# Kernel optimization log

Hardware: AMD Instinct MI355X
Metric: run time of the kernel (lower is better)

The kernel has to match this reference:

```python
import jax, jax.numpy as jnp
import numpy as np

EMBED = 1024
HEAD = 128

def setup_inputs() -> dict:
    key = jax.random.key(0)
    k1, k2, k3, k4 = jax.random.split(key, 4)
    x = jax.random.normal(k1, (4, 4096, EMBED), dtype=jnp.float32)
    # nn.Linear default init ~ U(-1/sqrt(fan_in), 1/sqrt(fan_in)); weights stored as [in, out] for x @ W
    s = 1.0 / np.sqrt(EMBED)
    Wq = jax.random.uniform(k2, (EMBED, HEAD), dtype=jnp.float32, minval=-s, maxval=s)
    Wk = jax.random.uniform(k3, (EMBED, HEAD), dtype=jnp.float32, minval=-s, maxval=s)
    Wv = jax.random.uniform(k4, (EMBED, HEAD), dtype=jnp.float32, minval=-s, maxval=s)
    return {"x": x, "Wq": Wq, "Wk": Wk, "Wv": Wv}

def reference(x, Wq, Wk, Wv):
    # x: [B, S, E]
    B, S, E = x.shape
    q = x @ Wq  # [B, S, H]
    k = x @ Wk
    v = x @ Wv
    scale = jnp.asarray(k.shape[-1], x.dtype) ** -0.5
    scores = jnp.einsum('bqh,bkh->bqk', q, k) * scale  # [B, S, S]
    causal = jnp.tril(jnp.ones((S, S), dtype=bool))
    scores = jnp.where(causal, scores, jnp.asarray(-jnp.inf, x.dtype))
    attn = jax.nn.softmax(scores, axis=-1)
    return jnp.einsum('bqk,bkh->bqh', attn, v)  # [B, S, H]
```

## Files before the change

### kernel.cpp

```cpp
#include <hip/hip_runtime.h>
#include <math.h>

#define BATCH 4
#define SEQ   4096
#define EMB   1024
#define HD    128
#define MROWS (BATCH*SEQ)
#define SCALE  0.08838834764831844f
#define SCALEQ 0.12751742f
#define CHUNK 10
#define NJOBS 119
#define MAXC  7

typedef __attribute__((ext_vector_type(8))) short bf16x8;
typedef __attribute__((ext_vector_type(4))) short short4v;
typedef __attribute__((ext_vector_type(4))) float f32x4;
typedef __attribute__((ext_vector_type(4))) int   i32x4;
typedef __attribute__((ext_vector_type(2))) int   i32x2;

static __device__ __forceinline__ unsigned short f2bf(float f) {
    unsigned int u = __float_as_uint(f);
    u += 0x7fff + ((u >> 16) & 1);
    return (unsigned short)(u >> 16);
}
static __device__ __forceinline__ float bf2f(unsigned short s) {
    return __uint_as_float((unsigned int)s << 16);
}
static __device__ __forceinline__ short4v pack4(float4 a) {
    short4v p;
    p[0] = (short)f2bf(a.x); p[1] = (short)f2bf(a.y);
    p[2] = (short)f2bf(a.z); p[3] = (short)f2bf(a.w);
    return p;
}
static __device__ __forceinline__ int cvtpk(float lo, float hi) {
    int r;
    asm("v_cvt_pk_bf16_f32 %0, %1, %2" : "=v"(r) : "v"(lo), "v"(hi));
    return r;
}
static __device__ __forceinline__ void gload_lds16(const unsigned short* g, unsigned short* l) {
    __builtin_amdgcn_global_load_lds(
        (const __attribute__((address_space(1))) void*)g,
        (__attribute__((address_space(3))) void*)l, 16, 0, 0);
}

__global__ __launch_bounds__(256) void wtrans_kernel(
    const float* __restrict__ Wq, const float* __restrict__ Wk,
    const float* __restrict__ Wv, unsigned short* __restrict__ Wt)
{
    __shared__ __align__(16) unsigned short Xs[16 * 132];
    const int w  = blockIdx.y;
    const float* W = (w == 0) ? Wq : (w == 1) ? Wk : Wv;
    const float sc = (w == 0) ? SCALEQ : 1.0f;
    const int bx = blockIdx.x;
    const int k0 = bx * 16;
    const int t  = threadIdx.x;

#pragma unroll
    for (int i = 0; i < 2; ++i) {
        int gg = i * 256 + t;
        int row = gg >> 5, c4 = gg & 31;
        float4 a = *(const float4*)&W[(size_t)(k0 + row) * HD + c4 * 4];
        short4v p;
        p[0] = (short)f2bf(a.x * sc); p[1] = (short)f2bf(a.y * sc);
        p[2] = (short)f2bf(a.z * sc); p[3] = (short)f2bf(a.w * sc);
        *(short4v*)&Xs[row * 132 + c4 * 4] = p;
    }
    __syncthreads();
    const int n = t >> 1, g = t & 1;
    i32x4 o;
#pragma unroll
    for (int e = 0; e < 4; ++e) {
        unsigned int lo = Xs[(g * 8 + e * 2    ) * 132 + n];
        unsigned int hi = Xs[(g * 8 + e * 2 + 1) * 132 + n];
        o[e] = (int)(lo | (hi << 16));
    }
    const int ntg  = w * 8 + (n >> 4);
    const int kc   = bx >> 1;
    const int quad = (bx * 2 + g) & 3;
    const int lane = quad * 16 + (n & 15);
    *(i32x4*)&Wt[(((size_t)ntg * 32 + kc) * 64 + lane) * 8] = o;
}

__global__ __launch_bounds__(512, 2) void qkv_kernel(
    const float* __restrict__ x, const unsigned short* __restrict__ Wt,
    unsigned short* __restrict__ qb, unsigned short* __restrict__ kb,
    unsigned short* __restrict__ vtb)
{
    __shared__ __align__(1024) unsigned short lds[58368];
    unsigned short* Ws  = lds;
    unsigned short* xsA = lds + 49152;
    unsigned short* xsB = lds + 53760;

    const int t    = threadIdx.x;
    const int lane = t & 63, ng = t >> 6;
    const int quad = lane >> 4, l16 = lane & 15;
    const int m0   = blockIdx.x * 64;

    f32x4 acc[4][3];
#pragma unroll
    for (int i = 0; i < 4; ++i)
#pragma unroll
        for (int j = 0; j < 3; ++j) acc[i][j] = (f32x4){0.f, 0.f, 0.f, 0.f};

    const int xr0 = t >> 4,         xc0 = (t & 15) * 4;
    const int xr1 = (t + 512) >> 4, xc1 = ((t + 512) & 15) * 4;
    const float* xb0 = x + (size_t)(m0 + xr0) * EMB + xc0;
    const float* xb1 = x + (size_t)(m0 + xr1) * EMB + xc1;

    const unsigned short* Wg = Wt + (size_t)lane * 8;
    float4 xra, xrb;

    {
        float4 a = *(const float4*)&xb0[0];
        float4 b = *(const float4*)&xb1[0];
        *(short4v*)&xsA[xr0 * 72 + xc0] = pack4(a);
        *(short4v*)&xsA[xr1 * 72 + xc1] = pack4(b);
#pragma unroll
        for (int jt = 0; jt < 3; ++jt)
#pragma unroll
            for (int kcl = 0; kcl < 2; ++kcl) {
                int ntg = ng * 3 + jt;
                gload_lds16(Wg + ((size_t)ntg * 32 + kcl) * 512,
                            Ws + ((size_t)ntg * 2 + kcl) * 512);
            }
        xra = *(const float4*)&xb0[64];
        xrb = *(const float4*)&xb1[64];
    }
    asm volatile("s_waitcnt vmcnt(2)" ::: "memory");
    asm volatile("s_waitcnt lgkmcnt(0)" ::: "memory");
    __builtin_amdgcn_s_barrier();

    for (int ph = 0; ph < 16; ++ph) {
        const int cb = ph & 1, nb = cb ^ 1;
        unsigned short* xc = cb ? xsB : xsA;
        unsigned short* xn = cb ? xsA : xsB;
        const int kcn = (ph < 15 ? ph + 1 : 15) * 2;

#pragma unroll
        for (int jt = 0; jt < 3; ++jt)
#pragma unroll
            for (int kcl = 0; kcl < 2; ++kcl) {
                int ntg = ng * 3 + jt;
                gload_lds16(Wg + ((size_t)ntg * 32 + kcn + kcl) * 512,
                            Ws + ((size_t)(nb * 48) + ntg * 2 + kcl) * 512);
            }
        *(short4v*)&xn[xr0 * 72 + xc0] = pack4(xra);
        *(short4v*)&xn[xr1 * 72 + xc1] = pack4(xrb);
        {
            const int xcol = (ph + 2 < 16) ? (ph + 2) * 64 : 960;
            xra = *(const float4*)&xb0[xcol];
            xrb = *(const float4*)&xb1[xcol];
        }
        {
            bf16x8 aA[2][4], aB[2][3];
#pragma unroll
            for (int ks = 0; ks < 2; ++ks)
#pragma unroll
                for (int jt = 0; jt < 3; ++jt)
                    aB[ks][jt] = *(const bf16x8*)&Ws[((size_t)(cb * 48) + (ng * 3 + jt) * 2 + ks) * 512 + lane * 8];
#pragma unroll
            for (int ks = 0; ks < 2; ++ks)
#pragma unroll
                for (int mt = 0; mt < 4; ++mt)
                    aA[ks][mt] = *(const bf16x8*)&xc[(mt * 16 + l16) * 72 + ks * 32 + quad * 8];
            __builtin_amdgcn_s_setprio(1);
#pragma unroll
            for (int ks = 0; ks < 2; ++ks)
#pragma unroll
                for (int mt = 0; mt < 4; ++mt)
#pragma unroll
                    for (int jt = 0; jt < 3; ++jt)
                        acc[mt][jt] = __builtin_amdgcn_mfma_f32_16x16x32_bf16(
                            aA[ks][mt], aB[ks][jt], acc[mt][jt], 0, 0, 0);
            __builtin_amdgcn_s_setprio(0);
        }
        asm volatile("s_waitcnt vmcnt(2)" ::: "memory");
        asm volatile("s_waitcnt lgkmcnt(0)" ::: "memory");
        __builtin_amdgcn_s_barrier();
    }

    unsigned short* Cq = lds;
    unsigned short* Ck = lds + 64 * 136;
    unsigned short* Cv = lds + 2 * 64 * 136;
#pragma unroll
    for (int mt = 0; mt < 4; ++mt)
#pragma unroll
        for (int jt = 0; jt < 3; ++jt) {
            int nt = ng * 3 + jt;
            int wm = nt >> 3, nl = nt & 7;
            if (wm < 2) {
                unsigned short* C = (wm == 0) ? Cq : Ck;
#pragma unroll
                for (int rr = 0; rr < 4; ++rr)
                    C[(mt * 16 + quad * 4 + rr) * 136 + nl * 16 + l16] =
                        f2bf(acc[mt][jt][rr]);
            } else {
                i32x2 p;
                p[0] = cvtpk(acc[mt][jt][0], acc[mt][jt][1]);
                p[1] = cvtpk(acc[mt][jt][2], acc[mt][jt][3]);
                *(i32x2*)&Cv[(nl * 16 + l16) * 72 + mt * 16 + quad * 4] = p;
            }
        }
    __syncthreads();
    {
#pragma unroll
        for (int i = 0; i < 2; ++i) {
            int idx = i * 512 + t;
            int row = idx >> 4, seg = idx & 15;
            *(i32x4*)&qb[((size_t)(m0 + row)) * HD + seg * 8] = *(const i32x4*)&Cq[row * 136 + seg * 8];
            *(i32x4*)&kb[((size_t)(m0 + row)) * HD + seg * 8] = *(const i32x4*)&Ck[row * 136 + seg * 8];
        }
    }
    {
        const int b = m0 >> 12, s0 = m0 & 4095;
#pragma unroll
        for (int i = 0; i < 2; ++i) {
            int idx = i * 512 + t;
            int h = idx >> 3, seg = idx & 7;
            *(i32x4*)&vtb[(size_t)b * (HD * SEQ) + (size_t)h * SEQ + s0 + seg * 8] =
                *(const i32x4*)&Cv[h * 72 + seg * 8];
        }
    }
}

#define PADK 136
#define PADV 72
#define PADP 72
#define DEFER_THR 8.0f

__global__ __launch_bounds__(512, 4) void flash_kernel(
    const unsigned short* __restrict__ qb, const unsigned short* __restrict__ kb,
    const unsigned short* __restrict__ vtb, unsigned short* __restrict__ Opart,
    float* __restrict__ mbuf, float* __restrict__ lbuf)
{
    __shared__ __align__(16) unsigned short Ks[64 * PADK];
    __shared__ __align__(16) unsigned short Vt[128 * PADV];
    __shared__ __align__(16) unsigned short Pt[128 * PADP];

    const int bx   = blockIdx.x;
    const int slot = bx & 7, pp = bx >> 3;
    const int b    = slot >> 1;
    const int jj   = pp * 2 + (slot & 1);
    if (jj >= NJOBS) return;

    const int t    = threadIdx.x;
    const int lane = t & 63, w = t >> 6;
    const int quad = lane >> 4, l16 = lane & 15;

    int qi = 0, s = 0;
    for (qi = 0; qi < 32; ++qi) {
        int cnt = (qi + 5) / 5;
        if (jj < s + cnt) break;
        s += cnt;
    }
    const int c    = jj - s;
    const int qrow = qi * 128 + w * 16 + l16;
    const int jmax = 2 * qi + 2;
    const int jbeg = c * CHUNK;
    const int jend = min(jbeg + CHUNK, jmax);
    const int wtop = qi * 128 + w * 16;

    bf16x8 qf[4];
    {
        const unsigned short* qp = qb + ((size_t)b * SEQ + qrow) * HD;
#pragma unroll
        for (int ks = 0; ks < 4; ++ks)
            qf[ks] = *(const bf16x8*)&qp[ks * 32 + quad * 8];
    }

    f32x4 O[8];
#pragma unroll
    for (int i = 0; i < 8; ++i) O[i] = (f32x4){0.f, 0.f, 0.f, 0.f};
    float m_run = -1e30f, l_run = 0.f;

    const unsigned short* kbb  = kb  + (size_t)b * SEQ * HD;
    const unsigned short* vtbb = vtb + (size_t)b * HD * SEQ;

    const int gg0 = t, gg1 = 512 + t;
    i32x4 kr0, kr1, vr0, vr1;
    kr0 = *(const i32x4*)&kbb[(size_t)jbeg * 64 * HD + (size_t)gg0 * 8];
    kr1 = *(const i32x4*)&kbb[(size_t)jbeg * 64 * HD + (size_t)gg1 * 8];
    vr0 = *(const i32x4*)&vtbb[(size_t)(gg0 >> 3) * SEQ + jbeg * 64 + (gg0 & 7) * 8];
    vr1 = *(const i32x4*)&vtbb[(size_t)(gg1 >> 3) * SEQ + jbeg * 64 + (gg1 & 7) * 8];

    for (int j0 = jbeg; j0 < jend; ++j0) {
        __syncthreads();
        *(i32x4*)&Ks[(gg0 >> 4) * PADK + (gg0 & 15) * 8] = kr0;
        *(i32x4*)&Ks[(gg1 >> 4) * PADK + (gg1 & 15) * 8] = kr1;
        *(i32x4*)&Vt[(gg0 >> 3) * PADV + (gg0 & 7) * 8] = vr0;
        *(i32x4*)&Vt[(gg1 >> 3) * PADV + (gg1 & 7) * 8] = vr1;
        __syncthreads();

        if (j0 + 1 < jend) {
            const int j1 = j0 + 1;
            kr0 = *(const i32x4*)&kbb[(size_t)j1 * 64 * HD + (size_t)gg0 * 8];
            kr1 = *(const i32x4*)&kbb[(size_t)j1 * 64 * HD + (size_t)gg1 * 8];
            vr0 = *(const i32x4*)&vtbb[(size_t)(gg0 >> 3) * SEQ + j1 * 64 + (gg0 & 7) * 8];
            vr1 = *(const i32x4*)&vtbb[(size_t)(gg1 >> 3) * SEQ + j1 * 64 + (gg1 & 7) * 8];
        }

        if (j0 * 64 > wtop + 15) continue;

        f32x4 st[4];
        __builtin_amdgcn_s_setprio(1);
#pragma unroll
        for (int mt = 0; mt < 4; ++mt) {
            f32x4 a = (f32x4){0.f, 0.f, 0.f, 0.f};
#pragma unroll
            for (int ks = 0; ks < 4; ++ks) {
                bf16x8 kf = *(const bf16x8*)&Ks[(mt * 16 + l16) * PADK + ks * 32 + quad * 8];
                a = __builtin_amdgcn_mfma_f32_16x16x32_bf16(kf, qf[ks], a, 0, 0, 0);
            }
            st[mt] = a;
        }
        __builtin_amdgcn_s_setprio(0);

        if (j0 * 64 + 63 > wtop) {
#pragma unroll
            for (int mt = 0; mt < 4; ++mt)
#pragma unroll
                for (int rr = 0; rr < 4; ++rr) {
                    int kv = j0 * 64 + mt * 16 + quad * 4 + rr;
                    if (kv > qrow) st[mt][rr] = -1e30f;
                }
        }

        float mx = -1e30f;
#pragma unroll
        for (int mt = 0; mt < 4; ++mt)
#pragma unroll
            for (int rr = 0; rr < 4; ++rr) mx = fmaxf(mx, st[mt][rr]);
        mx = fmaxf(mx, __shfl_xor(mx, 16));
        mx = fmaxf(mx, __shfl_xor(mx, 32));
        if (!__all(mx <= m_run + DEFER_THR)) {
            const float m_new = fmaxf(m_run, mx);
            const float alpha = exp2f(m_run - m_new);
            l_run *= alpha;
#pragma unroll
            for (int i = 0; i < 8; ++i) {
                O[i][0] *= alpha; O[i][1] *= alpha; O[i][2] *= alpha; O[i][3] *= alpha;
            }
            m_run = m_new;
        }
        float psum = 0.f;
#pragma unroll
        for (int mt = 0; mt < 4; ++mt)
#pragma unroll
            for (int rr = 0; rr < 4; ++rr) {
                float p = exp2f(st[mt][rr] - m_run);
                st[mt][rr] = p;
                psum += p;
            }
        psum += __shfl_xor(psum, 16);
        psum += __shfl_xor(psum, 32);
        l_run += psum;

#pragma unroll
        for (int mt = 0; mt < 4; ++mt) {
            i32x2 p;
            p[0] = cvtpk(st[mt][0], st[mt][1]);
            p[1] = cvtpk(st[mt][2], st[mt][3]);
            *(i32x2*)&Pt[(w * 16 + l16) * PADP + mt * 16 + quad * 4] = p;
        }

        bf16x8 pf0 = *(const bf16x8*)&Pt[(w * 16 + l16) * PADP + quad * 8];
        bf16x8 pf1 = *(const bf16x8*)&Pt[(w * 16 + l16) * PADP + 32 + quad * 8];
        __builtin_amdgcn_s_setprio(1);
#pragma unroll
        for (int mt = 0; mt < 8; ++mt) {
            bf16x8 vf0 = *(const bf16x8*)&Vt[(mt * 16 + l16) * PADV + quad * 8];
            bf16x8 vf1 = *(const bf16x8*)&Vt[(mt * 16 + l16) * PADV + 32 + quad * 8];
            O[mt] = __builtin_amdgcn_mfma_f32_16x16x32_bf16(vf0, pf0, O[mt], 0, 0, 0);
            O[mt] = __builtin_amdgcn_mfma_f32_16x16x32_bf16(vf1, pf1, O[mt], 0, 0, 0);
        }
        __builtin_amdgcn_s_setprio(0);
    }

    const int r = w * 16 + l16;
    const size_t jobbase = (size_t)b * NJOBS + jj;
    unsigned short* po = Opart + jobbase * (128 * 128) + (size_t)r * 128;
#pragma unroll
    for (int mt = 0; mt < 8; ++mt) {
        i32x2 p;
        p[0] = cvtpk(O[mt][0], O[mt][1]);
        p[1] = cvtpk(O[mt][2], O[mt][3]);
        *(i32x2*)&po[mt * 16 + quad * 4] = p;
    }
    if (quad == 0) {
        mbuf[jobbase * 128 + r] = m_run;
        lbuf[jobbase * 128 + r] = l_run;
    }
}

__global__ __launch_bounds__(512) void combine_kernel(
    const unsigned short* __restrict__ Opart, const float* __restrict__ mbuf,
    const float* __restrict__ lbuf, float* __restrict__ out)
{
    const int qi = blockIdx.x, b = blockIdx.y;
    const int nc = (qi + 5) / 5;
    int j0 = 0;
    for (int q = 0; q < qi; ++q) j0 += (q + 5) / 5;
    const int t = threadIdx.x;
    const int row = t >> 2, cg = (t & 3) * 32;

    float mv[MAXC], lv[MAXC];
    float M = -1e30f;
#pragma unroll
    for (int c2 = 0; c2 < MAXC; ++c2) {
        if (c2 < nc) {
            const size_t jb = (size_t)b * NJOBS + j0 + c2;
            mv[c2] = mbuf[jb * 128 + row];
            lv[c2] = lbuf[jb * 128 + row];
            M = fmaxf(M, mv[c2]);
        } else { mv[c2] = -1e30f; lv[c2] = 0.f; }
    }
    float L = 0.f;
#pragma unroll
    for (int c2 = 0; c2 < MAXC; ++c2)
        if (c2 < nc) L += exp2f(mv[c2] - M) * lv[c2];
    const float Linv = 1.0f / L;

    float acc[32];
#pragma unroll
    for (int i = 0; i < 32; ++i) acc[i] = 0.f;
#pragma unroll
    for (int c2 = 0; c2 < MAXC; ++c2) {
        if (c2 < nc) {
            const float wgt = exp2f(mv[c2] - M) * Linv;
            const unsigned short* po = Opart + ((size_t)b * NJOBS + j0 + c2) * (128 * 128) +
                                       (size_t)row * 128 + cg;
#pragma unroll
            for (int i = 0; i < 4; ++i) {
                i32x4 d = *(const i32x4*)&po[i * 8];
#pragma unroll
                for (int e = 0; e < 4; ++e) {
                    unsigned int u = (unsigned int)d[e];
                    acc[i * 8 + e * 2]     = fmaf(wgt, bf2f((unsigned short)(u & 0xffff)), acc[i * 8 + e * 2]);
                    acc[i * 8 + e * 2 + 1] = fmaf(wgt, bf2f((unsigned short)(u >> 16)),   acc[i * 8 + e * 2 + 1]);
                }
            }
        }
    }
    float* op = out + ((size_t)b * SEQ + qi * 128 + row) * HD + cg;
#pragma unroll
    for (int i = 0; i < 8; ++i) {
        float4 res;
        res.x = acc[i * 4]; res.y = acc[i * 4 + 1];
        res.z = acc[i * 4 + 2]; res.w = acc[i * 4 + 3];
        *(float4*)&op[i * 4] = res;
    }
}

extern "C" void kernel_launch(void* const* d_in, const int* in_sizes, int n_in,
                              void* d_out, int out_size, void* d_ws, size_t ws_size,
                              hipStream_t stream) {
    const float* x  = (const float*)d_in[0];
    const float* Wq = (const float*)d_in[1];
    const float* Wk = (const float*)d_in[2];
    const float* Wv = (const float*)d_in[3];

    unsigned short* qb    = (unsigned short*)d_ws;
    unsigned short* kb    = qb  + (size_t)MROWS * HD;
    unsigned short* vtb   = kb  + (size_t)MROWS * HD;
    unsigned short* Wt    = vtb + (size_t)MROWS * HD;
    unsigned short* Opart = Wt  + (size_t)3 * HD * EMB;
    float* mbuf = (float*)(Opart + (size_t)BATCH * NJOBS * 128 * 128);
    float* lbuf = mbuf + (size_t)BATCH * NJOBS * 128;
    float* out = (float*)d_out;

    wtrans_kernel <<<dim3(64, 3),  dim3(256), 0, stream>>>(Wq, Wk, Wv, Wt);
    qkv_kernel    <<<dim3(256),    dim3(512), 0, stream>>>(x, Wt, qb, kb, vtb);
    flash_kernel  <<<dim3(480),    dim3(512), 0, stream>>>(qb, kb, vtb, Opart, mbuf, lbuf);
    combine_kernel<<<dim3(32, 4),  dim3(512), 0, stream>>>(Opart, mbuf, lbuf, out);
}
```

Measured before the change: 169.0 us.

## Shrink flash query tile to 64 rows with 256-thread blocks and rebalance chunking

Reduces each flash-attention work item from 128 query rows (8 waves) to 64 query rows (4 waves). Blocks become 256 threads, and the split-KV job table is recomputed with CHUNK 12 and a new count formula, giving 204 jobs per batch instead of 119. The K/V tile loads are spread over four vectors per thread, and the combine kernel and workspace layout are resized to match. The goal is more blocks and better load balance across CUs, at the cost of each K/V tile being reused by fewer query rows and more partial outputs to combine.

```diff
diff --git a/kernel.cpp b/kernel.cpp
--- a/kernel.cpp
+++ b/kernel.cpp
@@ -8,9 +8,9 @@
 #define MROWS (BATCH*SEQ)
 #define SCALE  0.08838834764831844f
 #define SCALEQ 0.12751742f
-#define CHUNK 10
-#define NJOBS 119
-#define MAXC  7
+#define CHUNK 12
+#define NJOBS 204
+#define MAXC  6
 
 typedef __attribute__((ext_vector_type(8))) short bf16x8;
 typedef __attribute__((ext_vector_type(4))) short short4v;
@@ -228,19 +228,19 @@
 #define PADP 72
 #define DEFER_THR 8.0f
 
-__global__ __launch_bounds__(512, 4) void flash_kernel(
+__global__ __launch_bounds__(256, 3) void flash_kernel(
     const unsigned short* __restrict__ qb, const unsigned short* __restrict__ kb,
     const unsigned short* __restrict__ vtb, unsigned short* __restrict__ Opart,
     float* __restrict__ mbuf, float* __restrict__ lbuf)
 {
     __shared__ __align__(16) unsigned short Ks[64 * PADK];
     __shared__ __align__(16) unsigned short Vt[128 * PADV];
-    __shared__ __align__(16) unsigned short Pt[128 * PADP];
+    __shared__ __align__(16) unsigned short Pt[64 * PADP];
 
     const int bx   = blockIdx.x;
-    const int slot = bx & 7, pp = bx >> 3;
+    const int slot = bx & 7;
     const int b    = slot >> 1;
-    const int jj   = pp * 2 + (slot & 1);
+    const int jj   = (bx >> 3) * 2 + (slot & 1);
     if (jj >= NJOBS) return;
 
     const int t    = threadIdx.x;
@@ -248,17 +248,17 @@
     const int quad = lane >> 4, l16 = lane & 15;
 
     int qi = 0, s = 0;
-    for (qi = 0; qi < 32; ++qi) {
-        int cnt = (qi + 5) / 5;
+    for (qi = 0; qi < 64; ++qi) {
+        int cnt = (qi + 12) / 12;
         if (jj < s + cnt) break;
         s += cnt;
     }
     const int c    = jj - s;
-    const int qrow = qi * 128 + w * 16 + l16;
-    const int jmax = 2 * qi + 2;
+    const int qrow = qi * 64 + w * 16 + l16;
+    const int jmax = qi + 1;
     const int jbeg = c * CHUNK;
     const int jend = min(jbeg + CHUNK, jmax);
-    const int wtop = qi * 128 + w * 16;
+    const int wtop = qi * 64 + w * 16;
 
     bf16x8 qf[4];
     {
@@ -276,27 +276,32 @@
     const unsigned short* kbb  = kb  + (size_t)b * SEQ * HD;
     const unsigned short* vtbb = vtb + (size_t)b * HD * SEQ;
 
-    const int gg0 = t, gg1 = 512 + t;
-    i32x4 kr0, kr1, vr0, vr1;
-    kr0 = *(const i32x4*)&kbb[(size_t)jbeg * 64 * HD + (size_t)gg0 * 8];
-    kr1 = *(const i32x4*)&kbb[(size_t)jbeg * 64 * HD + (size_t)gg1 * 8];
-    vr0 = *(const i32x4*)&vtbb[(size_t)(gg0 >> 3) * SEQ + jbeg * 64 + (gg0 & 7) * 8];
-    vr1 = *(const i32x4*)&vtbb[(size_t)(gg1 >> 3) * SEQ + jbeg * 64 + (gg1 & 7) * 8];
+    i32x4 kr[4], vr[4];
+#pragma unroll
+    for (int i = 0; i < 4; ++i) {
+        int gg = i * 256 + t;
+        kr[i] = *(const i32x4*)&kbb[(size_t)jbeg * 64 * HD + (size_t)gg * 8];
+        vr[i] = *(const i32x4*)&vtbb[(size_t)(gg >> 3) * SEQ + jbeg * 64 + (gg & 7) * 8];
+    }
 
     for (int j0 = jbeg; j0 < jend; ++j0) {
         __syncthreads();
-        *(i32x4*)&Ks[(gg0 >> 4) * PADK + (gg0 & 15) * 8] = kr0;
-        *(i32x4*)&Ks[(gg1 >> 4) * PADK + (gg1 & 15) * 8] = kr1;
-        *(i32x4*)&Vt[(gg0 >> 3) * PADV + (gg0 & 7) * 8] = vr0;
-        *(i32x4*)&Vt[(gg1 >> 3) * PADV + (gg1 & 7) * 8] = vr1;
+#pragma unroll
+        for (int i = 0; i < 4; ++i) {
+            int gg = i * 256 + t;
+            *(i32x4*)&Ks[(gg >> 4) * PADK + (gg & 15) * 8] = kr[i];
+            *(i32x4*)&Vt[(gg >> 3) * PADV + (gg & 7) * 8] = vr[i];
+        }
         __syncthreads();
 
         if (j0 + 1 < jend) {
             const int j1 = j0 + 1;
-            kr0 = *(const i32x4*)&kbb[(size_t)j1 * 64 * HD + (size_t)gg0 * 8];
-            kr1 = *(const i32x4*)&kbb[(size_t)j1 * 64 * HD + (size_t)gg1 * 8];
-            vr0 = *(const i32x4*)&vtbb[(size_t)(gg0 >> 3) * SEQ + j1 * 64 + (gg0 & 7) * 8];
-            vr1 = *(const i32x4*)&vtbb[(size_t)(gg1 >> 3) * SEQ + j1 * 64 + (gg1 & 7) * 8];
+#pragma unroll
+            for (int i = 0; i < 4; ++i) {
+                int gg = i * 256 + t;
+                kr[i] = *(const i32x4*)&kbb[(size_t)j1 * 64 * HD + (size_t)gg * 8];
+                vr[i] = *(const i32x4*)&vtbb[(size_t)(gg >> 3) * SEQ + j1 * 64 + (gg & 7) * 8];
+            }
         }
 
         if (j0 * 64 > wtop + 15) continue;
@@ -378,7 +383,7 @@
 
     const int r = w * 16 + l16;
     const size_t jobbase = (size_t)b * NJOBS + jj;
-    unsigned short* po = Opart + jobbase * (128 * 128) + (size_t)r * 128;
+    unsigned short* po = Opart + jobbase * (64 * 128) + (size_t)r * 128;
 #pragma unroll
     for (int mt = 0; mt < 8; ++mt) {
         i32x2 p;
@@ -387,19 +392,19 @@
         *(i32x2*)&po[mt * 16 + quad * 4] = p;
     }
     if (quad == 0) {
-        mbuf[jobbase * 128 + r] = m_run;
-        lbuf[jobbase * 128 + r] = l_run;
-    }
-}
-
-__global__ __launch_bounds__(512) void combine_kernel(
+        mbuf[jobbase * 64 + r] = m_run;
+        lbuf[jobbase * 64 + r] = l_run;
+    }
+}
+
+__global__ __launch_bounds__(256) void combine_kernel(
     const unsigned short* __restrict__ Opart, const float* __restrict__ mbuf,
     const float* __restrict__ lbuf, float* __restrict__ out)
 {
     const int qi = blockIdx.x, b = blockIdx.y;
-    const int nc = (qi + 5) / 5;
+    const int nc = (qi + 12) / 12;
     int j0 = 0;
-    for (int q = 0; q < qi; ++q) j0 += (q + 5) / 5;
+    for (int q = 0; q < qi; ++q) j0 += (q + 12) / 12;
     const int t = threadIdx.x;
     const int row = t >> 2, cg = (t & 3) * 32;
 
@@ -409,8 +414,8 @@
     for (int c2 = 0; c2 < MAXC; ++c2) {
         if (c2 < nc) {
             const size_t jb = (size_t)b * NJOBS + j0 + c2;
-            mv[c2] = mbuf[jb * 128 + row];
-            lv[c2] = lbuf[jb * 128 + row];
+            mv[c2] = mbuf[jb * 64 + row];
+            lv[c2] = lbuf[jb * 64 + row];
             M = fmaxf(M, mv[c2]);
         } else { mv[c2] = -1e30f; lv[c2] = 0.f; }
     }
@@ -427,7 +432,7 @@
     for (int c2 = 0; c2 < MAXC; ++c2) {
         if (c2 < nc) {
             const float wgt = exp2f(mv[c2] - M) * Linv;
-            const unsigned short* po = Opart + ((size_t)b * NJOBS + j0 + c2) * (128 * 128) +
+            const unsigned short* po = Opart + ((size_t)b * NJOBS + j0 + c2) * (64 * 128) +
                                        (size_t)row * 128 + cg;
 #pragma unroll
             for (int i = 0; i < 4; ++i) {
@@ -441,7 +446,7 @@
             }
         }
     }
-    float* op = out + ((size_t)b * SEQ + qi * 128 + row) * HD + cg;
+    float* op = out + ((size_t)b * SEQ + qi * 64 + row) * HD + cg;
 #pragma unroll
     for (int i = 0; i < 8; ++i) {
         float4 res;
@@ -464,12 +469,12 @@
     unsigned short* vtb   = kb  + (size_t)MROWS * HD;
     unsigned short* Wt    = vtb + (size_t)MROWS * HD;
     unsigned short* Opart = Wt  + (size_t)3 * HD * EMB;
-    float* mbuf = (float*)(Opart + (size_t)BATCH * NJOBS * 128 * 128);
-    float* lbuf = mbuf + (size_t)BATCH * NJOBS * 128;
+    float* mbuf = (float*)(Opart + (size_t)BATCH * NJOBS * 64 * 128);
+    float* lbuf = mbuf + (size_t)BATCH * NJOBS * 64;
     float* out = (float*)d_out;
 
     wtrans_kernel <<<dim3(64, 3),  dim3(256), 0, stream>>>(Wq, Wk, Wv, Wt);
     qkv_kernel    <<<dim3(256),    dim3(512), 0, stream>>>(x, Wt, qb, kb, vtb);
-    flash_kernel  <<<dim3(480),    dim3(512), 0, stream>>>(qb, kb, vtb, Opart, mbuf, lbuf);
-    combine_kernel<<<dim3(32, 4),  dim3(512), 0, stream>>>(Opart, mbuf, lbuf, out);
-}
+    flash_kernel  <<<dim3(816),    dim3(256), 0, stream>>>(qb, kb, vtb, Opart, mbuf, lbuf);
+    combine_kernel<<<dim3(64, 4),  dim3(256), 0, stream>>>(Opart, mbuf, lbuf, out);
+}
```

New measurement: 176.1 us. 4.2% more time.

## Fuse split-KV combine into flash kernel via last-block atomic counter

Applied to the files above, without the earlier changes.

Removes the separate combine kernel launch. Each flash block bumps a per-(batch, query-tile) atomic counter after writing its partial output, and the block that arrives last performs the merge and writes the final output. This saves a kernel launch and the tail gap between the two kernels, and lets the merges overlap with other flash work. In exchange it adds a memset, threadfences and an atomic per block, and the merge work now lands on the flash kernel's tail.

```diff
diff --git a/kernel.cpp b/kernel.cpp
--- a/kernel.cpp
+++ b/kernel.cpp
@@ -231,11 +231,13 @@
 __global__ __launch_bounds__(512, 4) void flash_kernel(
     const unsigned short* __restrict__ qb, const unsigned short* __restrict__ kb,
     const unsigned short* __restrict__ vtb, unsigned short* __restrict__ Opart,
-    float* __restrict__ mbuf, float* __restrict__ lbuf)
+    float* __restrict__ mbuf, float* __restrict__ lbuf,
+    unsigned int* __restrict__ ctr, float* __restrict__ out)
 {
     __shared__ __align__(16) unsigned short Ks[64 * PADK];
     __shared__ __align__(16) unsigned short Vt[128 * PADV];
     __shared__ __align__(16) unsigned short Pt[128 * PADP];
+    __shared__ int lastFlag;
 
     const int bx   = blockIdx.x;
     const int slot = bx & 7, pp = bx >> 3;
@@ -254,6 +256,7 @@
         s += cnt;
     }
     const int c    = jj - s;
+    const int nc   = (qi + 5) / 5;
     const int qrow = qi * 128 + w * 16 + l16;
     const int jmax = 2 * qi + 2;
     const int jbeg = c * CHUNK;
@@ -390,64 +393,66 @@
         mbuf[jobbase * 128 + r] = m_run;
         lbuf[jobbase * 128 + r] = l_run;
     }
-}
-
-__global__ __launch_bounds__(512) void combine_kernel(
-    const unsigned short* __restrict__ Opart, const float* __restrict__ mbuf,
-    const float* __restrict__ lbuf, float* __restrict__ out)
-{
-    const int qi = blockIdx.x, b = blockIdx.y;
-    const int nc = (qi + 5) / 5;
-    int j0 = 0;
-    for (int q = 0; q < qi; ++q) j0 += (q + 5) / 5;
-    const int t = threadIdx.x;
-    const int row = t >> 2, cg = (t & 3) * 32;
-
-    float mv[MAXC], lv[MAXC];
-    float M = -1e30f;
-#pragma unroll
-    for (int c2 = 0; c2 < MAXC; ++c2) {
-        if (c2 < nc) {
-            const size_t jb = (size_t)b * NJOBS + j0 + c2;
-            mv[c2] = mbuf[jb * 128 + row];
-            lv[c2] = lbuf[jb * 128 + row];
-            M = fmaxf(M, mv[c2]);
-        } else { mv[c2] = -1e30f; lv[c2] = 0.f; }
-    }
-    float L = 0.f;
-#pragma unroll
-    for (int c2 = 0; c2 < MAXC; ++c2)
-        if (c2 < nc) L += exp2f(mv[c2] - M) * lv[c2];
-    const float Linv = 1.0f / L;
-
-    float acc[32];
-#pragma unroll
-    for (int i = 0; i < 32; ++i) acc[i] = 0.f;
-#pragma unroll
-    for (int c2 = 0; c2 < MAXC; ++c2) {
-        if (c2 < nc) {
-            const float wgt = exp2f(mv[c2] - M) * Linv;
-            const unsigned short* po = Opart + ((size_t)b * NJOBS + j0 + c2) * (128 * 128) +
-                                       (size_t)row * 128 + cg;
-#pragma unroll
-            for (int i = 0; i < 4; ++i) {
-                i32x4 d = *(const i32x4*)&po[i * 8];
-#pragma unroll
-                for (int e = 0; e < 4; ++e) {
-                    unsigned int u = (unsigned int)d[e];
-                    acc[i * 8 + e * 2]     = fmaf(wgt, bf2f((unsigned short)(u & 0xffff)), acc[i * 8 + e * 2]);
-                    acc[i * 8 + e * 2 + 1] = fmaf(wgt, bf2f((unsigned short)(u >> 16)),   acc[i * 8 + e * 2 + 1]);
+
+    __threadfence();
+    __syncthreads();
+    if (t == 0) {
+        unsigned int old = atomicAdd(&ctr[b * 32 + qi], 1u);
+        lastFlag = (old == (unsigned)(nc - 1));
+    }
+    __syncthreads();
+    if (!lastFlag) return;
+    __threadfence();
+
+    {
+        const int row = t >> 2, cg = (t & 3) * 32;
+        const int j0b = s;
+        float mv[MAXC], lv[MAXC];
+        float M = -1e30f;
+#pragma unroll
+        for (int c2 = 0; c2 < MAXC; ++c2) {
+            if (c2 < nc) {
+                const size_t jb = (size_t)b * NJOBS + j0b + c2;
+                mv[c2] = mbuf[jb * 128 + row];
+                lv[c2] = lbuf[jb * 128 + row];
+                M = fmaxf(M, mv[c2]);
+            } else { mv[c2] = -1e30f; lv[c2] = 0.f; }
+        }
+        float L = 0.f;
+#pragma unroll
+        for (int c2 = 0; c2 < MAXC; ++c2)
+            if (c2 < nc) L += exp2f(mv[c2] - M) * lv[c2];
+        const float Linv = 1.0f / L;
+
+        float acc[32];
+#pragma unroll
+        for (int i = 0; i < 32; ++i) acc[i] = 0.f;
+#pragma unroll
+        for (int c2 = 0; c2 < MAXC; ++c2) {
+            if (c2 < nc) {
+                const float wgt = exp2f(mv[c2] - M) * Linv;
+                const unsigned short* pp2 = Opart + ((size_t)b * NJOBS + j0b + c2) * (128 * 128) +
+                                            (size_t)row * 128 + cg;
+#pragma unroll
+                for (int i = 0; i < 4; ++i) {
+                    i32x4 d = *(const i32x4*)&pp2[i * 8];
+#pragma unroll
+                    for (int e = 0; e < 4; ++e) {
+                        unsigned int u = (unsigned int)d[e];
+                        acc[i * 8 + e * 2]     = fmaf(wgt, bf2f((unsigned short)(u & 0xffff)), acc[i * 8 + e * 2]);
+                        acc[i * 8 + e * 2 + 1] = fmaf(wgt, bf2f((unsigned short)(u >> 16)),   acc[i * 8 + e * 2 + 1]);
+                    }
                 }
             }
         }
-    }
-    float* op = out + ((size_t)b * SEQ + qi * 128 + row) * HD + cg;
-#pragma unroll
-    for (int i = 0; i < 8; ++i) {
-        float4 res;
-        res.x = acc[i * 4]; res.y = acc[i * 4 + 1];
-        res.z = acc[i * 4 + 2]; res.w = acc[i * 4 + 3];
-        *(float4*)&op[i * 4] = res;
+        float* op = out + ((size_t)b * SEQ + qi * 128 + row) * HD + cg;
+#pragma unroll
+        for (int i = 0; i < 8; ++i) {
+            float4 res;
+            res.x = acc[i * 4]; res.y = acc[i * 4 + 1];
+            res.z = acc[i * 4 + 2]; res.w = acc[i * 4 + 3];
+            *(float4*)&op[i * 4] = res;
+        }
     }
 }
 
@@ -466,10 +471,11 @@
     unsigned short* Opart = Wt  + (size_t)3 * HD * EMB;
     float* mbuf = (float*)(Opart + (size_t)BATCH * NJOBS * 128 * 128);
     float* lbuf = mbuf + (size_t)BATCH * NJOBS * 128;
+    unsigned int* ctr = (unsigned int*)(lbuf + (size_t)BATCH * NJOBS * 128);
     float* out = (float*)d_out;
 
+    hipMemsetAsync(ctr, 0, BATCH * 32 * sizeof(unsigned int), stream);
     wtrans_kernel <<<dim3(64, 3),  dim3(256), 0, stream>>>(Wq, Wk, Wv, Wt);
     qkv_kernel    <<<dim3(256),    dim3(512), 0, stream>>>(x, Wt, qb, kb, vtb);
-    flash_kernel  <<<dim3(480),    dim3(512), 0, stream>>>(qb, kb, vtb, Opart, mbuf, lbuf);
-    combine_kernel<<<dim3(32, 4),  dim3(512), 0, stream>>>(Opart, mbuf, lbuf, out);
-}
+    flash_kernel  <<<dim3(480),    dim3(512), 0, stream>>>(qb, kb, vtb, Opart, mbuf, lbuf, ctr, out);
+}
```

After: 347.3 us. 105% more time.
